# Kernel tuning notes

Measured on AMD Instinct MI355X. Metric: run time of the kernel, lower is better.

The kernel has to match this reference:

```python
import jax, jax.numpy as jnp
import numpy as np

N_CELLS = 500_000
B = 512
D_X = 128
D_Z = 32
D_IN = D_X + D_Z  # 160
H = 256
D_OUT = 16


def _linear_params(key, fan_in, fan_out):
    k1, k2 = jax.random.split(key)
    bound = 1.0 / np.sqrt(fan_in)
    W = jax.random.uniform(k1, (fan_in, fan_out), jnp.float32, -bound, bound)
    b = jax.random.uniform(k2, (fan_out,), jnp.float32, -bound, bound)
    return W, b


def setup_inputs() -> dict:
    key = jax.random.key(0)
    ks = jax.random.split(key, 8)
    X = jax.random.uniform(ks[0], (N_CELLS, D_X), jnp.float32)  # nonneg counts-like
    Z = jax.random.normal(ks[1], (B, D_Z), jnp.float32)
    cell_to_batch = jax.random.randint(ks[2], (N_CELLS,), 0, B, jnp.int64)
    sample_idx_batch = jnp.arange(B, dtype=jnp.int64)
    W1, b1 = _linear_params(ks[3], D_IN, H)
    W2, b2 = _linear_params(ks[4], H, H)
    W3, b3 = _linear_params(ks[5], H, D_OUT)
    return {"X": X, "Z": Z, "W1": W1, "b1": b1, "W2": W2, "b2": b2,
            "W3": W3, "b3": b3, "cell_to_batch": cell_to_batch,
            "sample_idx_batch": sample_idx_batch}


def reference(X, Z, W1, b1, W2, b2, W3, b3, cell_to_batch, sample_idx_batch):
    # gather per-sample covariates to per-cell rows
    Zc = Z[cell_to_batch]                              # [N, D_Z]
    seg = sample_idx_batch[cell_to_batch]              # [N] remapped sample ids
    # preprocessor: log-normalize X, concat covariates
    Xp = jnp.concatenate([jnp.log1p(X), Zc], axis=-1)  # [N, D_IN]
    # cell predictor MLP (Linear-ReLU x2 + Linear)
    h = jax.nn.relu(Xp @ W1 + b1)
    h = jax.nn.relu(h @ W2 + b2)
    X_cell = h @ W3 + b3                               # [N, D_OUT]
    # aggregator: segment mean over cells of each sample
    nseg = sample_idx_batch.shape[0]
    sums = jax.ops.segment_sum(X_cell, seg, num_segments=nseg)
    counts = jax.ops.segment_sum(jnp.ones((X_cell.shape[0], 1), X_cell.dtype), seg, num_segments=nseg)
    Y_sample = sums / jnp.maximum(counts, 1.0)
    # postprocessor: identity
    return Y_sample
```

## Files before the change

### kernel.cpp

```cpp
#include <hip/hip_runtime.h>
#include <hip/hip_bf16.h>

typedef __attribute__((ext_vector_type(8))) short short8;
typedef __attribute__((ext_vector_type(4))) float floatx4;

#define N_CELLS  500000
#define B_SAMP   512
#define D_X      128
#define D_Z      32
#define D_IN     160
#define H_DIM    256
#define D_OUT    16

#define M_TILE   32
#define LDA      168
#define LDH      264

#define OFF_W1P   0
#define OFF_W2P   81920
#define OFF_W3P   212992
#define OFF_XCELL 221184
#define OFF_PART  32221184
#define N_CHUNK   256
#define PART_STRIDE 8704

__global__ void pack_w(const float* __restrict__ W, __hip_bfloat16* __restrict__ dst,
                       int N, int kS) {
    int idx = blockIdx.x * blockDim.x + threadIdx.x;
    int j = idx & 7;
    int L = (idx >> 3) & 63;
    int s = (idx >> 9) % kS;
    int t = idx / (kS << 9);
    int k = s * 32 + ((L >> 4) << 3) + j;
    int n = t * 16 + (L & 15);
    dst[idx] = __float2bfloat16(W[(size_t)k * N + n]);
}

__global__ __launch_bounds__(256, 3)
void fused_mlp(const float* __restrict__ X, const float* __restrict__ Z,
               const int* __restrict__ c2b,
               const float* __restrict__ b1, const float* __restrict__ b2,
               const float* __restrict__ b3,
               const __hip_bfloat16* __restrict__ w1p,
               const __hip_bfloat16* __restrict__ w2p,
               const __hip_bfloat16* __restrict__ w3p,
               float* __restrict__ xcell) {
    __shared__ __hip_bfloat16 sXp[M_TILE][LDA];
    __shared__ __hip_bfloat16 sH[2][M_TILE][LDH];
    __shared__ float sP[4][M_TILE][D_OUT];

    const int tid = threadIdx.x;
    const int w   = tid >> 6;
    const int L   = tid & 63;
    const int q   = L >> 4;
    const int ln  = L & 15;
    const int base = blockIdx.x * M_TILE;

#pragma unroll
    for (int i = 0; i < 4; ++i) {
        int idx = tid + i * 256;
        int row = idx >> 5;
        int c4  = idx & 31;
        float4 v = *(const float4*)(X + (size_t)(base + row) * D_X + c4 * 4);
        __hip_bfloat16* d = &sXp[row][c4 * 4];
        d[0] = __float2bfloat16(__logf(1.0f + v.x));
        d[1] = __float2bfloat16(__logf(1.0f + v.y));
        d[2] = __float2bfloat16(__logf(1.0f + v.z));
        d[3] = __float2bfloat16(__logf(1.0f + v.w));
    }
    {
        int row = tid >> 3;
        int c0  = (tid & 7) * 4;
        int b   = c2b[base + row];
        float4 v = *(const float4*)(Z + (size_t)b * D_Z + c0);
        __hip_bfloat16* d = &sXp[row][D_X + c0];
        d[0] = __float2bfloat16(v.x);
        d[1] = __float2bfloat16(v.y);
        d[2] = __float2bfloat16(v.z);
        d[3] = __float2bfloat16(v.w);
    }
    __syncthreads();

    floatx4 acc[2][4];
#pragma unroll
    for (int mt = 0; mt < 2; ++mt)
#pragma unroll
        for (int nt = 0; nt < 4; ++nt)
            acc[mt][nt] = (floatx4){0.f, 0.f, 0.f, 0.f};

    float bias1[4];
#pragma unroll
    for (int nt = 0; nt < 4; ++nt) bias1[nt] = b1[w * 64 + nt * 16 + ln];

#pragma unroll
    for (int s = 0; s < 5; ++s) {
        short8 a0 = *(const short8*)&sXp[ln][s * 32 + q * 8];
        short8 a1 = *(const short8*)&sXp[16 + ln][s * 32 + q * 8];
#pragma unroll
        for (int nt = 0; nt < 4; ++nt) {
            int t = w * 4 + nt;
            short8 bf = *(const short8*)(w1p + (size_t)(((t * 5 + s) << 6) + L) * 8);
            acc[0][nt] = __builtin_amdgcn_mfma_f32_16x16x32_bf16(a0, bf, acc[0][nt], 0, 0, 0);
            acc[1][nt] = __builtin_amdgcn_mfma_f32_16x16x32_bf16(a1, bf, acc[1][nt], 0, 0, 0);
        }
    }
#pragma unroll
    for (int mt = 0; mt < 2; ++mt)
#pragma unroll
        for (int nt = 0; nt < 4; ++nt)
#pragma unroll
            for (int r = 0; r < 4; ++r) {
                float v = fmaxf(acc[mt][nt][r] + bias1[nt], 0.0f);
                sH[0][mt * 16 + q * 4 + r][w * 64 + nt * 16 + ln] = __float2bfloat16(v);
            }
    __syncthreads();

#pragma unroll
    for (int mt = 0; mt < 2; ++mt)
#pragma unroll
        for (int nt = 0; nt < 4; ++nt)
            acc[mt][nt] = (floatx4){0.f, 0.f, 0.f, 0.f};

    float bias2[4];
#pragma unroll
    for (int nt = 0; nt < 4; ++nt) bias2[nt] = b2[w * 64 + nt * 16 + ln];

#pragma unroll
    for (int s = 0; s < 8; ++s) {
        short8 a0 = *(const short8*)&sH[0][ln][s * 32 + q * 8];
        short8 a1 = *(const short8*)&sH[0][16 + ln][s * 32 + q * 8];
#pragma unroll
        for (int nt = 0; nt < 4; ++nt) {
            int t = w * 4 + nt;
            short8 bf = *(const short8*)(w2p + (size_t)(((t * 8 + s) << 6) + L) * 8);
            acc[0][nt] = __builtin_amdgcn_mfma_f32_16x16x32_bf16(a0, bf, acc[0][nt], 0, 0, 0);
            acc[1][nt] = __builtin_amdgcn_mfma_f32_16x16x32_bf16(a1, bf, acc[1][nt], 0, 0, 0);
        }
    }
#pragma unroll
    for (int mt = 0; mt < 2; ++mt)
#pragma unroll
        for (int nt = 0; nt < 4; ++nt)
#pragma unroll
            for (int r = 0; r < 4; ++r) {
                float v = fmaxf(acc[mt][nt][r] + bias2[nt], 0.0f);
                sH[1][mt * 16 + q * 4 + r][w * 64 + nt * 16 + ln] = __float2bfloat16(v);
            }
    __syncthreads();

    floatx4 acc3[2];
    acc3[0] = (floatx4){0.f, 0.f, 0.f, 0.f};
    acc3[1] = (floatx4){0.f, 0.f, 0.f, 0.f};
#pragma unroll
    for (int ss = 0; ss < 2; ++ss) {
        int s = w * 2 + ss;
        short8 a0 = *(const short8*)&sH[1][ln][s * 32 + q * 8];
        short8 a1 = *(const short8*)&sH[1][16 + ln][s * 32 + q * 8];
        short8 bf = *(const short8*)(w3p + (size_t)((s << 6) + L) * 8);
        acc3[0] = __builtin_amdgcn_mfma_f32_16x16x32_bf16(a0, bf, acc3[0], 0, 0, 0);
        acc3[1] = __builtin_amdgcn_mfma_f32_16x16x32_bf16(a1, bf, acc3[1], 0, 0, 0);
    }
#pragma unroll
    for (int mt = 0; mt < 2; ++mt)
#pragma unroll
        for (int r = 0; r < 4; ++r)
            sP[w][mt * 16 + q * 4 + r][ln] = acc3[mt][r];
    __syncthreads();

#pragma unroll
    for (int i = 0; i < 2; ++i) {
        int idx = tid + i * 256;
        int m = idx >> 4, n = idx & 15;
        float v = sP[0][m][n] + sP[1][m][n] + sP[2][m][n] + sP[3][m][n] + b3[n];
        xcell[(size_t)(base + m) * D_OUT + n] = v;
    }
}

__global__ __launch_bounds__(256)
void reduce_seg(const float* __restrict__ xcell, const int* __restrict__ c2b,
                const int* __restrict__ sidx, float* __restrict__ part) {
    __shared__ float ls[B_SAMP * D_OUT];
    __shared__ float lc[B_SAMP];
    const int tid = threadIdx.x;
    for (int i = tid; i < B_SAMP * D_OUT; i += 256) ls[i] = 0.f;
    for (int i = tid; i < B_SAMP; i += 256) lc[i] = 0.f;
    __syncthreads();

    const int cpc = (N_CELLS + N_CHUNK - 1) / N_CHUNK;
    const int start = blockIdx.x * cpc;
    const int end = min(start + cpc, N_CELLS);
    const int ci = tid >> 4;
    const int n  = tid & 15;
    for (int c = start + ci; c < end; c += 16) {
        int b = c2b[c];
        int s = sidx[b] & (B_SAMP - 1);
        float v = xcell[(size_t)c * D_OUT + n];
        atomicAdd(&ls[s * D_OUT + n], v);
        if (n == 0) atomicAdd(&lc[s], 1.0f);
    }
    __syncthreads();

    float* dst = part + (size_t)blockIdx.x * PART_STRIDE;
    for (int i = tid; i < B_SAMP * D_OUT; i += 256) dst[i] = ls[i];
    for (int i = tid; i < B_SAMP; i += 256) dst[B_SAMP * D_OUT + i] = lc[i];
}

__global__ __launch_bounds__(256)
void finalize(const float* __restrict__ part, float* __restrict__ out) {
    int o = blockIdx.x * blockDim.x + threadIdx.x;
    int s = o >> 4;
    float sum = 0.f, cnt = 0.f;
    for (int c = 0; c < N_CHUNK; ++c) {
        sum += part[(size_t)c * PART_STRIDE + o];
        cnt += part[(size_t)c * PART_STRIDE + B_SAMP * D_OUT + s];
    }
    out[o] = sum / fmaxf(cnt, 1.0f);
}

extern "C" void kernel_launch(void* const* d_in, const int* in_sizes, int n_in,
                              void* d_out, int out_size, void* d_ws, size_t ws_size,
                              hipStream_t stream) {
    const float* X   = (const float*)d_in[0];
    const float* Z   = (const float*)d_in[1];
    const float* W1  = (const float*)d_in[2];
    const float* b1  = (const float*)d_in[3];
    const float* W2  = (const float*)d_in[4];
    const float* b2  = (const float*)d_in[5];
    const float* W3  = (const float*)d_in[6];
    const float* b3  = (const float*)d_in[7];
    const int*   c2b = (const int*)d_in[8];
    const int*   sidx= (const int*)d_in[9];

    char* ws = (char*)d_ws;
    __hip_bfloat16* w1p = (__hip_bfloat16*)(ws + OFF_W1P);
    __hip_bfloat16* w2p = (__hip_bfloat16*)(ws + OFF_W2P);
    __hip_bfloat16* w3p = (__hip_bfloat16*)(ws + OFF_W3P);
    float* xcell = (float*)(ws + OFF_XCELL);
    float* part  = (float*)(ws + OFF_PART);
    float* out   = (float*)d_out;

    pack_w<<<160, 256, 0, stream>>>(W1, w1p, H_DIM, 5);
    pack_w<<<256, 256, 0, stream>>>(W2, w2p, H_DIM, 8);
    pack_w<<<16,  256, 0, stream>>>(W3, w3p, D_OUT, 8);

    fused_mlp<<<N_CELLS / M_TILE, 256, 0, stream>>>(X, Z, c2b, b1, b2, b3,
                                                    w1p, w2p, w3p, xcell);
    reduce_seg<<<N_CHUNK, 256, 0, stream>>>(xcell, c2b, sidx, part);
    finalize<<<32, 256, 0, stream>>>(part, out);
}
```

Baseline: 562.9 us.

## Fuse segment reduction into MLP kernel via replicated global atomics

Removes the intermediate per-cell output buffer and the separate reduction kernel. Each MLP block now atomically adds its outputs and counts into one of 64 replicated global accumulators. Finalize sums the replicas. This avoids writing and rereading the per-cell buffer, at the cost of global atomic traffic and an extra zeroing kernel.

```diff
diff --git a/kernel.cpp b/kernel.cpp
--- a/kernel.cpp
+++ b/kernel.cpp
@@ -16,13 +16,13 @@
 #define LDA      168
 #define LDH      264
 
+#define NREP     64
+
 #define OFF_W1P   0
 #define OFF_W2P   81920
 #define OFF_W3P   212992
-#define OFF_XCELL 221184
-#define OFF_PART  32221184
-#define N_CHUNK   256
-#define PART_STRIDE 8704
+#define OFF_ACC   221184
+#define OFF_CNT   2318336
 
 __global__ void pack_w(const float* __restrict__ W, __hip_bfloat16* __restrict__ dst,
                        int N, int kS) {
@@ -36,15 +36,20 @@
     dst[idx] = __float2bfloat16(W[(size_t)k * N + n]);
 }
 
+__global__ void zero_ws(float* __restrict__ p, int n) {
+    int i = blockIdx.x * blockDim.x + threadIdx.x;
+    if (i < n) p[i] = 0.0f;
+}
+
 __global__ __launch_bounds__(256, 3)
 void fused_mlp(const float* __restrict__ X, const float* __restrict__ Z,
-               const int* __restrict__ c2b,
+               const int* __restrict__ c2b, const int* __restrict__ sidx,
                const float* __restrict__ b1, const float* __restrict__ b2,
                const float* __restrict__ b3,
                const __hip_bfloat16* __restrict__ w1p,
                const __hip_bfloat16* __restrict__ w2p,
                const __hip_bfloat16* __restrict__ w3p,
-               float* __restrict__ xcell) {
+               float* __restrict__ accs, float* __restrict__ cnts) {
     __shared__ __hip_bfloat16 sXp[M_TILE][LDA];
     __shared__ __hip_bfloat16 sH[2][M_TILE][LDH];
     __shared__ float sP[4][M_TILE][D_OUT];
@@ -167,52 +172,30 @@
             sP[w][mt * 16 + q * 4 + r][ln] = acc3[mt][r];
     __syncthreads();
 
+    float* accR = accs + (size_t)(blockIdx.x & (NREP - 1)) * (B_SAMP * D_OUT);
+    float* cntR = cnts + (size_t)(blockIdx.x & (NREP - 1)) * B_SAMP;
 #pragma unroll
     for (int i = 0; i < 2; ++i) {
         int idx = tid + i * 256;
         int m = idx >> 4, n = idx & 15;
         float v = sP[0][m][n] + sP[1][m][n] + sP[2][m][n] + sP[3][m][n] + b3[n];
-        xcell[(size_t)(base + m) * D_OUT + n] = v;
+        int b = c2b[base + m];
+        int s = sidx[b];
+        atomicAdd(&accR[(size_t)s * D_OUT + n], v);
+        if (n == 0) atomicAdd(&cntR[s], 1.0f);
     }
 }
 
 __global__ __launch_bounds__(256)
-void reduce_seg(const float* __restrict__ xcell, const int* __restrict__ c2b,
-                const int* __restrict__ sidx, float* __restrict__ part) {
-    __shared__ float ls[B_SAMP * D_OUT];
-    __shared__ float lc[B_SAMP];
-    const int tid = threadIdx.x;
-    for (int i = tid; i < B_SAMP * D_OUT; i += 256) ls[i] = 0.f;
-    for (int i = tid; i < B_SAMP; i += 256) lc[i] = 0.f;
-    __syncthreads();
-
-    const int cpc = (N_CELLS + N_CHUNK - 1) / N_CHUNK;
-    const int start = blockIdx.x * cpc;
-    const int end = min(start + cpc, N_CELLS);
-    const int ci = tid >> 4;
-    const int n  = tid & 15;
-    for (int c = start + ci; c < end; c += 16) {
-        int b = c2b[c];
-        int s = sidx[b] & (B_SAMP - 1);
-        float v = xcell[(size_t)c * D_OUT + n];
-        atomicAdd(&ls[s * D_OUT + n], v);
-        if (n == 0) atomicAdd(&lc[s], 1.0f);
-    }
-    __syncthreads();
-
-    float* dst = part + (size_t)blockIdx.x * PART_STRIDE;
-    for (int i = tid; i < B_SAMP * D_OUT; i += 256) dst[i] = ls[i];
-    for (int i = tid; i < B_SAMP; i += 256) dst[B_SAMP * D_OUT + i] = lc[i];
-}
-
-__global__ __launch_bounds__(256)
-void finalize(const float* __restrict__ part, float* __restrict__ out) {
+void finalize(const float* __restrict__ accs, const float* __restrict__ cnts,
+              float* __restrict__ out) {
     int o = blockIdx.x * blockDim.x + threadIdx.x;
     int s = o >> 4;
     float sum = 0.f, cnt = 0.f;
-    for (int c = 0; c < N_CHUNK; ++c) {
-        sum += part[(size_t)c * PART_STRIDE + o];
-        cnt += part[(size_t)c * PART_STRIDE + B_SAMP * D_OUT + s];
+#pragma unroll 8
+    for (int r = 0; r < NREP; ++r) {
+        sum += accs[(size_t)r * (B_SAMP * D_OUT) + o];
+        cnt += cnts[(size_t)r * B_SAMP + s];
     }
     out[o] = sum / fmaxf(cnt, 1.0f);
 }
@@ -235,16 +218,20 @@
     __hip_bfloat16* w1p = (__hip_bfloat16*)(ws + OFF_W1P);
     __hip_bfloat16* w2p = (__hip_bfloat16*)(ws + OFF_W2P);
     __hip_bfloat16* w3p = (__hip_bfloat16*)(ws + OFF_W3P);
-    float* xcell = (float*)(ws + OFF_XCELL);
-    float* part  = (float*)(ws + OFF_PART);
-    float* out   = (float*)d_out;
+    float* accs = (float*)(ws + OFF_ACC);
+    float* cnts = (float*)(ws + OFF_CNT);
+    float* out  = (float*)d_out;
+
+    {
+        int nz = NREP * (B_SAMP * D_OUT + B_SAMP);
+        zero_ws<<<(nz + 255) / 256, 256, 0, stream>>>(accs, nz);
+    }
 
     pack_w<<<160, 256, 0, stream>>>(W1, w1p, H_DIM, 5);
     pack_w<<<256, 256, 0, stream>>>(W2, w2p, H_DIM, 8);
     pack_w<<<16,  256, 0, stream>>>(W3, w3p, D_OUT, 8);
 
-    fused_mlp<<<N_CELLS / M_TILE, 256, 0, stream>>>(X, Z, c2b, b1, b2, b3,
-                                                    w1p, w2p, w3p, xcell);
-    reduce_seg<<<N_CHUNK, 256, 0, stream>>>(xcell, c2b, sidx, part);
-    finalize<<<32, 256, 0, stream>>>(part, out);
-}
+    fused_mlp<<<N_CELLS / M_TILE, 256, 0, stream>>>(X, Z, c2b, sidx, b1, b2, b3,
+                                                    w1p, w2p, w3p, accs, cnts);
+    finalize<<<32, 256, 0, stream>>>(accs, cnts, out);
+}
```

Result: faster. 510.6 us (-9.3%).
